# Optimization experiments

Hardware: AMD Instinct MI355X
Metric: run time of the kernel (lower is better)

## Reference

```python
import jax, jax.numpy as jnp
import numpy as np

# ---- static module configuration (mirrors __init__) ----
BIG, SMALL = 13, 3
IN_C = 256
GHOST_RATIO = 0.23
NK = -(-BIG // SMALL)                          # ceil(13/3) = 5 small kernels tile the big one
REP_N = int(IN_C * (1 - GHOST_RATIO)) // 2 * 2 # 196 channels go through the big-kernel path
GHOST_N = IN_C - REP_N                         # 60 identity (ghost) channels
OUT_N = REP_N * NK                             # grouped conv channel-multiplier output
PAD = SMALL - 1                                # conv padding = 2 -> conv output is (H+2, W+2)
CROP = SMALL // 2                              # crop to emulate padding=k//2 on the small axis
MID = BIG // 2
REAL_PAD = [MID - i * SMALL - PAD for i in range(NK)]  # [4, 1, -2, -5, -8] shift offsets
P = BIG                                        # safe zero-pad for static shift slicing
N_PATH = 2
BN_EPS = 1e-5


def _split_indices():
    # exact replication of the module's fixed random ghost/rep channel split
    np.random.seed(123)
    ghost = np.sort(np.random.choice(IN_C, GHOST_N, replace=False))
    rep = np.sort(np.array(list(set(range(IN_C)) - set(ghost.tolist())), dtype=np.int64))
    return jnp.asarray(ghost, jnp.int32), jnp.asarray(rep, jnp.int32)


def _dwconv(x, w):
    # depthwise conv with channel multiplier NK: groups = REP_N
    return jax.lax.conv_general_dilated(
        x, w, window_strides=(1, 1), padding=[(PAD, PAD), (PAD, PAD)],
        dimension_numbers=('NCHW', 'OIHW', 'NCHW'), feature_group_count=REP_N)


def _bn(x, g, b):
    # BatchNorm2d in training mode (batch statistics), matching nn.(Sync)BatchNorm forward
    m = jnp.mean(x, axis=(0, 2, 3), keepdims=True)
    v = jnp.var(x, axis=(0, 2, 3), keepdims=True)
    return (x - m) * jax.lax.rsqrt(v + BN_EPS) * g[None, :, None, None] + b[None, :, None, None]


def setup_inputs() -> dict:
    key = jax.random.key(0)
    ks = jax.random.split(key, 4)
    B, H, W = 32, 56, 56
    inputs = jax.random.normal(ks[0], (B, IN_C, H, W), jnp.float32)
    fan = SMALL * SMALL  # groups=REP_N -> in_ch/groups = 1
    std = (2.0 / fan) ** 0.5
    w1 = jax.random.normal(ks[1], (OUT_N, 1, SMALL, SMALL), jnp.float32) * std
    w2 = jax.random.normal(ks[2], (OUT_N, 1, SMALL, SMALL), jnp.float32) * std
    ghost_idx, rep_idx = _split_indices()
    ones = jnp.ones((REP_N,), jnp.float32)
    zeros = jnp.zeros((REP_N,), jnp.float32)
    return {
        'inputs': inputs, 'w1': w1, 'w2': w2,
        'g1': ones, 'b1': zeros, 'g2': ones, 'b2': zeros, 'g3': ones, 'b3': zeros,
        'ghost_idx': ghost_idx, 'rep_idx': rep_idx,
    }


def reference(inputs, w1, w2, g1, b1, g2, b2, g3, b3, ghost_idx, rep_idx):
    B, C, H, W = inputs.shape
    rep_x = jnp.take(inputs, rep_idx, axis=1)      # [B, REP_N, H, W]
    ghost_x = jnp.take(inputs, ghost_idx, axis=1)  # [B, GHOST_N, H, W]

    # N_path grouped depthwise convs summed (pre-merge branch of the module)
    out = _dwconv(rep_x, w1) + _dwconv(rep_x, w2)  # [B, REP_N*NK, H+2, W+2]
    H2, W2 = out.shape[-2:]
    # grouped conv channel order: channel c -> outputs c*NK .. c*NK+NK-1
    x = out.reshape(B, REP_N, NK, H2, W2)

    # AddShift: stack the NK small-conv responses with shifts to emulate
    # a (BIG x SMALL) kernel (shift along H) and a (SMALL x BIG) kernel (shift along W).
    lora1 = jnp.zeros((B, REP_N, H, W), out.dtype)
    lora2 = jnp.zeros((B, REP_N, H, W), out.dtype)
    for i, r in enumerate(REAL_PAD):  # NK is a small static constant
        ci = x[:, :, i]  # [B, REP_N, H2, W2]
        yh = jnp.pad(ci, ((0, 0), (0, 0), (P, P), (0, 0)))
        lora1 = lora1 + yh[:, :, P - r:P - r + H, CROP:CROP + W]
        yw = jnp.pad(ci, ((0, 0), (0, 0), (0, 0), (P, P)))
        lora2 = lora2 + yw[:, :, CROP:CROP + H, P - r:P - r + W]
    # small-kernel branch: center chunk, cropped to emulate padding=SMALL//2
    small = x[:, :, NK // 2, CROP:CROP + H, CROP:CROP + W]

    y = _bn(lora1, g1, b1) + _bn(lora2, g2, b2) + _bn(small, g3, b3) + rep_x
    return jnp.concatenate([y, ghost_x], axis=1)  # [B, IN_C, H, W]
```

## Files before the change

### kernel.cpp

```cpp
#include <hip/hip_runtime.h>


#define LSTRIDE 76
#define LROWS 70
#define LDS_FLOATS (LROWS * LSTRIDE)

__device__ __forceinline__ void load_tile(float* tile, const float* __restrict__ src, int tid) {
  #pragma unroll 1
  for (int g = tid; g < LDS_FLOATS / 4; g += 256)
    reinterpret_cast<float4*>(tile)[g] = float4{0.f, 0.f, 0.f, 0.f};
  __syncthreads();
  #pragma unroll 1
  for (int g = tid; g < 784; g += 256) {
    float4 v = reinterpret_cast<const float4*>(src)[g];
    int r = g / 14, c4 = g - r * 14;
    float* p = &tile[(r + 6) * LSTRIDE + 10 + 4 * c4];
    reinterpret_cast<float2*>(p)[0] = float2{v.x, v.y};
    reinterpret_cast<float2*>(p)[1] = float2{v.z, v.w};
  }
  __syncthreads();
}

__device__ __forceinline__ void conv_lora1(
    const float* tile, const float* wv, int h0, int w0,
    float (&a1)[4][4], float (&xc)[4][4]) {
  #pragma unroll
  for (int rr = 0; rr < 18; ++rr) {
    const float* rp = &tile[(h0 + rr) * LSTRIDE + w0 + 8];
    const float4 qa = *reinterpret_cast<const float4*>(rp);
    const float4 qb = *reinterpret_cast<const float4*>(rp + 4);
    const float xr[8] = {qa.x, qa.y, qa.z, qa.w, qb.x, qb.y, qb.z, qb.w};
    if (rr >= 6 && rr < 10) {
      #pragma unroll
      for (int dw = 0; dw < 4; ++dw) xc[rr - 6][dw] = xr[dw + 2];
    }
    #pragma unroll
    for (int dh = 0; dh < 4; ++dh) {
      const int t = rr - dh;
      if (t >= 0 && t < 15) {
        #pragma unroll
        for (int kw = 0; kw < 3; ++kw) {
          const float wgt = wv[3 * t + kw];
          #pragma unroll
          for (int dw = 0; dw < 4; ++dw)
            a1[dh][dw] = fmaf(xr[dw + kw + 1], wgt, a1[dh][dw]);
        }
      }
    }
  }
}

__device__ __forceinline__ void conv_l2s(
    const float* tile, const float* wv, int h0, int w0,
    float (&a2)[4][4], float (&a3)[4][4]) {
  #pragma unroll
  for (int rr = 0; rr < 6; ++rr) {
    const float* rp = &tile[(h0 + 5 + rr) * LSTRIDE + w0 + 4];
    #pragma unroll
    for (int g = 0; g < 5; ++g) {
      const float4 q = reinterpret_cast<const float4*>(rp)[g];
      const float xq[4] = {q.x, q.y, q.z, q.w};
      #pragma unroll
      for (int v = 0; v < 4; ++v) {
        const int vv = 4 * g + v;
        #pragma unroll
        for (int dh = 0; dh < 4; ++dh) {
          const int kh = rr - dh;
          if (kh >= 0 && kh < 3) {
            #pragma unroll
            for (int dw = 0; dw < 4; ++dw) {
              const int t = vv - dw;
              if (t >= 0 && t < 15)
                a2[dh][dw] = fmaf(xq[v], wv[(t / 3) * 9 + kh * 3 + (t % 3)], a2[dh][dw]);
              const int kw2 = vv - 5 - dw;
              if (kw2 >= 0 && kw2 < 3)
                a3[dh][dw] = fmaf(xq[v], wv[18 + kh * 3 + kw2], a3[dh][dw]);
            }
          }
        }
      }
    }
  }
}

extern "C" __global__ void sw_prep(const float* __restrict__ w1, const float* __restrict__ w2,
                                   float* __restrict__ wsum) {
  int i = blockIdx.x * 256 + threadIdx.x;
  if (i < 8820) wsum[i] = w1[i] + w2[i];
}

extern "C" __global__ __launch_bounds__(256) void sw_pass1(
    const float* __restrict__ in, const int* __restrict__ rep_idx,
    const float* __restrict__ wsum, float* __restrict__ partial) {
  __shared__ float tile[LDS_FLOATS];
  __shared__ float red[4][6];
  const int bid = blockIdx.x;
  const int c = bid >> 5, b = bid & 31;
  const int tid = threadIdx.x;
  const int src_c = rep_idx[c];
  load_tile(tile, in + (size_t)(b * 256 + src_c) * 3136, tid);
  float wv[45];
  {
    const float* wp = wsum + c * 45;
    #pragma unroll
    for (int j = 0; j < 45; ++j) wv[j] = wp[j];
  }
  float s1 = 0, q1 = 0, s2 = 0, q2 = 0, s3 = 0, q3 = 0;
  if (tid < 196) {
    const int th = tid / 14, tw = tid - th * 14;
    const int h0 = th * 4, w0 = tw * 4;
    {
      float a1[4][4] = {}, xc[4][4];
      conv_lora1(tile, wv, h0, w0, a1, xc);
      #pragma unroll
      for (int dh = 0; dh < 4; ++dh)
        #pragma unroll
        for (int dw = 0; dw < 4; ++dw) { float v = a1[dh][dw]; s1 += v; q1 = fmaf(v, v, q1); }
    }
    {
      float a2[4][4] = {}, a3[4][4] = {};
      conv_l2s(tile, wv, h0, w0, a2, a3);
      #pragma unroll
      for (int dh = 0; dh < 4; ++dh)
        #pragma unroll
        for (int dw = 0; dw < 4; ++dw) {
          float v = a2[dh][dw]; s2 += v; q2 = fmaf(v, v, q2);
          float u = a3[dh][dw]; s3 += u; q3 = fmaf(u, u, q3);
        }
    }
  }
  #pragma unroll
  for (int off = 32; off > 0; off >>= 1) {
    s1 += __shfl_down(s1, off); q1 += __shfl_down(q1, off);
    s2 += __shfl_down(s2, off); q2 += __shfl_down(q2, off);
    s3 += __shfl_down(s3, off); q3 += __shfl_down(q3, off);
  }
  const int lane = tid & 63, wid = tid >> 6;
  if (lane == 0) {
    red[wid][0] = s1; red[wid][1] = q1; red[wid][2] = s2;
    red[wid][3] = q2; red[wid][4] = s3; red[wid][5] = q3;
  }
  __syncthreads();
  if (tid < 6)
    partial[bid * 6 + tid] = red[0][tid] + red[1][tid] + red[2][tid] + red[3][tid];
}

extern "C" __global__ void sw_reduce(
    const float* __restrict__ partial,
    const float* __restrict__ g1, const float* __restrict__ b1,
    const float* __restrict__ g2, const float* __restrict__ b2,
    const float* __restrict__ g3, const float* __restrict__ b3,
    float* __restrict__ stats2) {
  const int c = blockIdx.x;
  const int tid = threadIdx.x;
  __shared__ float sm[6];
  if (tid < 6) {
    float s = 0;
    for (int b = 0; b < 32; ++b) s += partial[(c * 32 + b) * 6 + tid];
    sm[tid] = s;
  }
  __syncthreads();
  if (tid == 0) {
    const float N = 100352.f;
    float m1 = sm[0] / N, v1 = sm[1] / N - m1 * m1;
    float m2 = sm[2] / N, v2 = sm[3] / N - m2 * m2;
    float m3 = sm[4] / N, v3 = sm[5] / N - m3 * m3;
    float A1 = g1[c] * rsqrtf(v1 + 1e-5f);
    float A2 = g2[c] * rsqrtf(v2 + 1e-5f);
    float A3 = g3[c] * rsqrtf(v3 + 1e-5f);
    float K = b1[c] + b2[c] + b3[c] - m1 * A1 - m2 * A2 - m3 * A3;
    stats2[c * 4 + 0] = A1; stats2[c * 4 + 1] = A2;
    stats2[c * 4 + 2] = A3; stats2[c * 4 + 3] = K;
  }
}

extern "C" __global__ __launch_bounds__(256) void sw_pass2(
    const float* __restrict__ in, const int* __restrict__ rep_idx,
    const int* __restrict__ ghost_idx, const float* __restrict__ wsum,
    const float* __restrict__ stats2, float* __restrict__ out) {
  const int bid = blockIdx.x;
  const int tid = threadIdx.x;
  if (bid >= 6272) {
    const int g2 = bid - 6272;
    const int j = g2 >> 5, b = g2 & 31;
    const int src_c = ghost_idx[j];
    const float4* s = reinterpret_cast<const float4*>(in + (size_t)(b * 256 + src_c) * 3136);
    float4* d = reinterpret_cast<float4*>(out + ((size_t)(b * 256) + 196 + j) * 3136);
    #pragma unroll 1
    for (int g = tid; g < 784; g += 256) d[g] = s[g];
    return;
  }
  __shared__ float tile[LDS_FLOATS];
  const int c = bid >> 5, b = bid & 31;
  const int src_c = rep_idx[c];
  load_tile(tile, in + (size_t)(b * 256 + src_c) * 3136, tid);
  float wv[45];
  {
    const float* wp = wsum + c * 45;
    #pragma unroll
    for (int j = 0; j < 45; ++j) wv[j] = wp[j];
  }
  const float A1 = stats2[c * 4 + 0], A2 = stats2[c * 4 + 1];
  const float A3 = stats2[c * 4 + 2], K = stats2[c * 4 + 3];
  if (tid < 196) {
    const int th = tid / 14, tw = tid - th * 14;
    const int h0 = th * 4, w0 = tw * 4;
    float y[4][4];
    {
      float a1[4][4] = {}, xc[4][4];
      conv_lora1(tile, wv, h0, w0, a1, xc);
      #pragma unroll
      for (int dh = 0; dh < 4; ++dh)
        #pragma unroll
        for (int dw = 0; dw < 4; ++dw)
          y[dh][dw] = fmaf(A1, a1[dh][dw], K + xc[dh][dw]);
    }
    {
      float a2[4][4] = {}, a3[4][4] = {};
      conv_l2s(tile, wv, h0, w0, a2, a3);
      #pragma unroll
      for (int dh = 0; dh < 4; ++dh)
        #pragma unroll
        for (int dw = 0; dw < 4; ++dw) {
          y[dh][dw] = fmaf(A2, a2[dh][dw], y[dh][dw]);
          y[dh][dw] = fmaf(A3, a3[dh][dw], y[dh][dw]);
        }
    }
    float* op = out + ((size_t)(b * 256) + c) * 3136;
    #pragma unroll
    for (int dh = 0; dh < 4; ++dh) {
      float4 o{y[dh][0], y[dh][1], y[dh][2], y[dh][3]};
      *reinterpret_cast<float4*>(op + (h0 + dh) * 56 + w0) = o;
    }
  }
}

extern "C" void kernel_launch(void* const* d_in, const int* in_sizes, int n_in,
                              void* d_out, int out_size, void* d_ws, size_t ws_size,
                              hipStream_t stream) {
  const float* in  = (const float*)d_in[0];
  const float* w1  = (const float*)d_in[1];
  const float* w2  = (const float*)d_in[2];
  const float* g1  = (const float*)d_in[3];
  const float* b1  = (const float*)d_in[4];
  const float* g2  = (const float*)d_in[5];
  const float* b2  = (const float*)d_in[6];
  const float* g3  = (const float*)d_in[7];
  const float* b3  = (const float*)d_in[8];
  const int* ghost_idx = (const int*)d_in[9];
  const int* rep_idx   = (const int*)d_in[10];
  float* out = (float*)d_out;
  float* ws  = (float*)d_ws;

  float* wsum    = ws;
  float* stats2  = ws + 8832;
  float* partial = ws + 9728;

  sw_prep<<<35, 256, 0, stream>>>(w1, w2, wsum);
  sw_pass1<<<6272, 256, 0, stream>>>(in, rep_idx, wsum, partial);
  sw_reduce<<<196, 64, 0, stream>>>(partial, g1, b1, g2, b2, g3, b3, stats2);
  sw_pass2<<<8192, 256, 0, stream>>>(in, rep_idx, ghost_idx, wsum, stats2, out);
}
```

Measured before the change: 182.7 us.

## Replace LDS tiles with register-streamed row windows over batch-parallel threads

The convolution kernels no longer stage a padded image tile in LDS. Each 448-thread block now covers 8 output rows of one channel across all 32 batch images, one thread per batch×4-column strip. Each thread streams 22 input rows straight from global memory into a register window, using clamped indices and masks for padding, and accumulates the vertical and horizontal branches in rolling register arrays. This removes the LDS zero-fill, barriers and per-image tile setup, and cuts the partial-sum count per channel to 7. In exchange it adds redundant global loads of overlapping halo rows, higher register pressure, and a single template kernel reused for both passes.

Result: faster. 170.4 us (-6.7%).

```diff
diff --git a/kernel.cpp b/kernel.cpp
--- a/kernel.cpp
+++ b/kernel.cpp
@@ -1,84 +1,183 @@
 #include <hip/hip_runtime.h>
 
 
-#define LSTRIDE 76
-#define LROWS 70
-#define LDS_FLOATS (LROWS * LSTRIDE)
-
-__device__ __forceinline__ void load_tile(float* tile, const float* __restrict__ src, int tid) {
-  #pragma unroll 1
-  for (int g = tid; g < LDS_FLOATS / 4; g += 256)
-    reinterpret_cast<float4*>(tile)[g] = float4{0.f, 0.f, 0.f, 0.f};
-  __syncthreads();
-  #pragma unroll 1
-  for (int g = tid; g < 784; g += 256) {
-    float4 v = reinterpret_cast<const float4*>(src)[g];
-    int r = g / 14, c4 = g - r * 14;
-    float* p = &tile[(r + 6) * LSTRIDE + 10 + 4 * c4];
-    reinterpret_cast<float2*>(p)[0] = float2{v.x, v.y};
-    reinterpret_cast<float2*>(p)[1] = float2{v.z, v.w};
-  }
-  __syncthreads();
-}
-
-__device__ __forceinline__ void conv_lora1(
-    const float* tile, const float* wv, int h0, int w0,
-    float (&a1)[4][4], float (&xc)[4][4]) {
+#define B_    32
+#define CIN   256
+#define REPN  196
+#define HW    56
+#define IMG   3136
+#define NTOT  (B_ * CIN * IMG)
+#define NCONVBLK 1400
+#define NGHOSTBLK 1920
+
+template <bool PASS2>
+__launch_bounds__(448)
+__global__ void sw_conv(const float* __restrict__ in, const int* __restrict__ rep_idx,
+                        const int* __restrict__ ghost_idx, const float* __restrict__ wsum,
+                        const float* __restrict__ stats2, float* __restrict__ partial,
+                        float* __restrict__ out) {
+  const int bid = blockIdx.x;
+  const int tid = threadIdx.x;
+
+  if (PASS2 && bid >= NCONVBLK) {
+    const int g = bid - NCONVBLK;
+    const int j = g >> 5, b = g & 31;
+    const int src_c = ghost_idx[j];
+    const float4* s = reinterpret_cast<const float4*>(in + (size_t)(b * CIN + src_c) * IMG);
+    float4* d = reinterpret_cast<float4*>(out + ((size_t)(b * CIN) + REPN + j) * IMG);
+    #pragma unroll 1
+    for (int i = tid; i < 784; i += 448) d[i] = s[i];
+    return;
+  }
+
+  const int c = (bid / 56) * 8 + (bid & 7);
+  const int rb = (bid % 56) >> 3;
+  if (c >= REPN) return;
+  const int h0 = rb * 8;
+
+  const int b = tid / 14;
+  const int tw = tid - b * 14;
+  const int w0 = tw * 4;
+  const int src_c = rep_idx[c];
+  const int ibase = (b * CIN + src_c) * IMG;
+
+  float wv[45];
   #pragma unroll
-  for (int rr = 0; rr < 18; ++rr) {
-    const float* rp = &tile[(h0 + rr) * LSTRIDE + w0 + 8];
-    const float4 qa = *reinterpret_cast<const float4*>(rp);
-    const float4 qb = *reinterpret_cast<const float4*>(rp + 4);
-    const float xr[8] = {qa.x, qa.y, qa.z, qa.w, qb.x, qb.y, qb.z, qb.w};
-    if (rr >= 6 && rr < 10) {
-      #pragma unroll
-      for (int dw = 0; dw < 4; ++dw) xc[rr - 6][dw] = xr[dw + 2];
-    }
+  for (int j = 0; j < 45; ++j) wv[j] = wsum[c * 45 + j];
+
+  float A1 = 0.f, A2 = 0.f, A3 = 0.f, K_ = 0.f;
+  if (PASS2) {
+    A1 = stats2[c * 4 + 0]; A2 = stats2[c * 4 + 1];
+    A3 = stats2[c * 4 + 2]; K_ = stats2[c * 4 + 3];
+  }
+
+  const float ma = (tw >= 2) ? 1.f : 0.f;
+  const float mb = (tw >= 1) ? 1.f : 0.f;
+  const float mc = (tw <= 12) ? 1.f : 0.f;
+  const float md = (tw <= 11) ? 1.f : 0.f;
+
+  float acc1[8][4] = {};
+  float acc2[3][4] = {};
+  float acc3[3][4] = {};
+  float stash[7][4];
+  float s1 = 0, q1 = 0, s2 = 0, q2 = 0, s3 = 0, q3 = 0;
+
+  #pragma unroll
+  for (int s = 0; s < 22; ++s) {
+    const int r = h0 - 6 + s;
+    if (r >= 0 && r < HW) {
+      float win[20];
+      {
+        const int base = ibase + r * HW + w0 - 8;
+        #pragma unroll
+        for (int g = 0; g < 5; ++g) {
+          int idx = base + 4 * g;
+          idx = idx < 0 ? 0 : idx;
+          idx = idx > (NTOT - 4) ? (NTOT - 4) : idx;
+          const float4 v = *reinterpret_cast<const float4*>(in + idx);
+          win[4 * g + 0] = v.x; win[4 * g + 1] = v.y;
+          win[4 * g + 2] = v.z; win[4 * g + 3] = v.w;
+        }
+      }
+      #pragma unroll
+      for (int e = 0; e < 4; ++e) win[e] *= ma;
+      #pragma unroll
+      for (int e = 4; e < 8; ++e) win[e] *= mb;
+      #pragma unroll
+      for (int e = 12; e < 16; ++e) win[e] *= mc;
+      #pragma unroll
+      for (int e = 16; e < 20; ++e) win[e] *= md;
+
+      #pragma unroll
+      for (int lr = 0; lr < 8; ++lr) {
+        const int t = s - lr;
+        if (t >= 0 && t < 15) {
+          #pragma unroll
+          for (int kw = 0; kw < 3; ++kw) {
+            const float wgt = wv[3 * t + kw];
+            #pragma unroll
+            for (int dw = 0; dw < 4; ++dw)
+              acc1[lr][dw] = fmaf(win[dw + kw + 7], wgt, acc1[lr][dw]);
+          }
+        }
+      }
+      #pragma unroll
+      for (int lr = 0; lr < 8; ++lr) {
+        const int kh = s - lr - 5;
+        if (kh >= 0 && kh < 3) {
+          #pragma unroll
+          for (int T = 0; T < 15; ++T) {
+            const float wgt = wv[(T / 3) * 9 + kh * 3 + (T % 3)];
+            #pragma unroll
+            for (int dw = 0; dw < 4; ++dw)
+              acc2[lr % 3][dw] = fmaf(win[dw + T + 2], wgt, acc2[lr % 3][dw]);
+          }
+          #pragma unroll
+          for (int kw = 0; kw < 3; ++kw) {
+            const float wgt = wv[18 + kh * 3 + kw];
+            #pragma unroll
+            for (int dw = 0; dw < 4; ++dw)
+              acc3[lr % 3][dw] = fmaf(win[dw + kw + 7], wgt, acc3[lr % 3][dw]);
+          }
+        }
+      }
+    }
+
+    if (s >= 14) {
+      const int lr = s - 14;
+      if (PASS2) {
+        const int hh = h0 + lr;
+        const float4 xv = *reinterpret_cast<const float4*>(in + ibase + hh * HW + w0);
+        float4 o;
+        o.x = fmaf(A1, acc1[lr][0], stash[lr % 7][0] + K_ + xv.x);
+        o.y = fmaf(A1, acc1[lr][1], stash[lr % 7][1] + K_ + xv.y);
+        o.z = fmaf(A1, acc1[lr][2], stash[lr % 7][2] + K_ + xv.z);
+        o.w = fmaf(A1, acc1[lr][3], stash[lr % 7][3] + K_ + xv.w);
+        *reinterpret_cast<float4*>(out + (size_t)(b * CIN + c) * IMG + hh * HW + w0) = o;
+      } else {
+        #pragma unroll
+        for (int dw = 0; dw < 4; ++dw) {
+          const float v = acc1[lr][dw];
+          s1 += v; q1 = fmaf(v, v, q1);
+        }
+      }
+    }
+    if (s >= 7 && s <= 14) {
+      const int lr = s - 7;
+      #pragma unroll
+      for (int dw = 0; dw < 4; ++dw) {
+        const float v2 = acc2[lr % 3][dw], v3 = acc3[lr % 3][dw];
+        if (PASS2) {
+          stash[lr % 7][dw] = fmaf(A2, v2, A3 * v3);
+        } else {
+          s2 += v2; q2 = fmaf(v2, v2, q2);
+          s3 += v3; q3 = fmaf(v3, v3, q3);
+        }
+        acc2[lr % 3][dw] = 0.f;
+        acc3[lr % 3][dw] = 0.f;
+      }
+    }
+  }
+
+  if (!PASS2) {
+    __shared__ float red[7][6];
     #pragma unroll
-    for (int dh = 0; dh < 4; ++dh) {
-      const int t = rr - dh;
-      if (t >= 0 && t < 15) {
-        #pragma unroll
-        for (int kw = 0; kw < 3; ++kw) {
-          const float wgt = wv[3 * t + kw];
-          #pragma unroll
-          for (int dw = 0; dw < 4; ++dw)
-            a1[dh][dw] = fmaf(xr[dw + kw + 1], wgt, a1[dh][dw]);
-        }
-      }
-    }
-  }
-}
-
-__device__ __forceinline__ void conv_l2s(
-    const float* tile, const float* wv, int h0, int w0,
-    float (&a2)[4][4], float (&a3)[4][4]) {
-  #pragma unroll
-  for (int rr = 0; rr < 6; ++rr) {
-    const float* rp = &tile[(h0 + 5 + rr) * LSTRIDE + w0 + 4];
-    #pragma unroll
-    for (int g = 0; g < 5; ++g) {
-      const float4 q = reinterpret_cast<const float4*>(rp)[g];
-      const float xq[4] = {q.x, q.y, q.z, q.w};
-      #pragma unroll
-      for (int v = 0; v < 4; ++v) {
-        const int vv = 4 * g + v;
-        #pragma unroll
-        for (int dh = 0; dh < 4; ++dh) {
-          const int kh = rr - dh;
-          if (kh >= 0 && kh < 3) {
-            #pragma unroll
-            for (int dw = 0; dw < 4; ++dw) {
-              const int t = vv - dw;
-              if (t >= 0 && t < 15)
-                a2[dh][dw] = fmaf(xq[v], wv[(t / 3) * 9 + kh * 3 + (t % 3)], a2[dh][dw]);
-              const int kw2 = vv - 5 - dw;
-              if (kw2 >= 0 && kw2 < 3)
-                a3[dh][dw] = fmaf(xq[v], wv[18 + kh * 3 + kw2], a3[dh][dw]);
-            }
-          }
-        }
-      }
+    for (int off = 32; off > 0; off >>= 1) {
+      s1 += __shfl_down(s1, off); q1 += __shfl_down(q1, off);
+      s2 += __shfl_down(s2, off); q2 += __shfl_down(q2, off);
+      s3 += __shfl_down(s3, off); q3 += __shfl_down(q3, off);
+    }
+    const int lane = tid & 63, wid = tid >> 6;
+    if (lane == 0) {
+      red[wid][0] = s1; red[wid][1] = q1; red[wid][2] = s2;
+      red[wid][3] = q2; red[wid][4] = s3; red[wid][5] = q3;
+    }
+    __syncthreads();
+    if (tid < 6) {
+      float t = 0;
+      #pragma unroll
+      for (int w = 0; w < 7; ++w) t += red[w][tid];
+      partial[(c * 7 + rb) * 6 + tid] = t;
     }
   }
 }
@@ -87,62 +186,6 @@
                                    float* __restrict__ wsum) {
   int i = blockIdx.x * 256 + threadIdx.x;
   if (i < 8820) wsum[i] = w1[i] + w2[i];
-}
-
-extern "C" __global__ __launch_bounds__(256) void sw_pass1(
-    const float* __restrict__ in, const int* __restrict__ rep_idx,
-    const float* __restrict__ wsum, float* __restrict__ partial) {
-  __shared__ float tile[LDS_FLOATS];
-  __shared__ float red[4][6];
-  const int bid = blockIdx.x;
-  const int c = bid >> 5, b = bid & 31;
-  const int tid = threadIdx.x;
-  const int src_c = rep_idx[c];
-  load_tile(tile, in + (size_t)(b * 256 + src_c) * 3136, tid);
-  float wv[45];
-  {
-    const float* wp = wsum + c * 45;
-    #pragma unroll
-    for (int j = 0; j < 45; ++j) wv[j] = wp[j];
-  }
-  float s1 = 0, q1 = 0, s2 = 0, q2 = 0, s3 = 0, q3 = 0;
-  if (tid < 196) {
-    const int th = tid / 14, tw = tid - th * 14;
-    const int h0 = th * 4, w0 = tw * 4;
-    {
-      float a1[4][4] = {}, xc[4][4];
-      conv_lora1(tile, wv, h0, w0, a1, xc);
-      #pragma unroll
-      for (int dh = 0; dh < 4; ++dh)
-        #pragma unroll
-        for (int dw = 0; dw < 4; ++dw) { float v = a1[dh][dw]; s1 += v; q1 = fmaf(v, v, q1); }
-    }
-    {
-      float a2[4][4] = {}, a3[4][4] = {};
-      conv_l2s(tile, wv, h0, w0, a2, a3);
-      #pragma unroll
-      for (int dh = 0; dh < 4; ++dh)
-        #pragma unroll
-        for (int dw = 0; dw < 4; ++dw) {
-          float v = a2[dh][dw]; s2 += v; q2 = fmaf(v, v, q2);
-          float u = a3[dh][dw]; s3 += u; q3 = fmaf(u, u, q3);
-        }
-    }
-  }
-  #pragma unroll
-  for (int off = 32; off > 0; off >>= 1) {
-    s1 += __shfl_down(s1, off); q1 += __shfl_down(q1, off);
-    s2 += __shfl_down(s2, off); q2 += __shfl_down(q2, off);
-    s3 += __shfl_down(s3, off); q3 += __shfl_down(q3, off);
-  }
-  const int lane = tid & 63, wid = tid >> 6;
-  if (lane == 0) {
-    red[wid][0] = s1; red[wid][1] = q1; red[wid][2] = s2;
-    red[wid][3] = q2; red[wid][4] = s3; red[wid][5] = q3;
-  }
-  __syncthreads();
-  if (tid < 6)
-    partial[bid * 6 + tid] = red[0][tid] + red[1][tid] + red[2][tid] + red[3][tid];
 }
 
 extern "C" __global__ void sw_reduce(
@@ -156,7 +199,8 @@
   __shared__ float sm[6];
   if (tid < 6) {
     float s = 0;
-    for (int b = 0; b < 32; ++b) s += partial[(c * 32 + b) * 6 + tid];
+    #pragma unroll
+    for (int rb = 0; rb < 7; ++rb) s += partial[(c * 7 + rb) * 6 + tid];
     sm[tid] = s;
   }
   __syncthreads();
@@ -171,67 +215,6 @@
     float K = b1[c] + b2[c] + b3[c] - m1 * A1 - m2 * A2 - m3 * A3;
     stats2[c * 4 + 0] = A1; stats2[c * 4 + 1] = A2;
     stats2[c * 4 + 2] = A3; stats2[c * 4 + 3] = K;
-  }
-}
-
-extern "C" __global__ __launch_bounds__(256) void sw_pass2(
-    const float* __restrict__ in, const int* __restrict__ rep_idx,
-    const int* __restrict__ ghost_idx, const float* __restrict__ wsum,
-    const float* __restrict__ stats2, float* __restrict__ out) {
-  const int bid = blockIdx.x;
-  const int tid = threadIdx.x;
-  if (bid >= 6272) {
-    const int g2 = bid - 6272;
-    const int j = g2 >> 5, b = g2 & 31;
-    const int src_c = ghost_idx[j];
-    const float4* s = reinterpret_cast<const float4*>(in + (size_t)(b * 256 + src_c) * 3136);
-    float4* d = reinterpret_cast<float4*>(out + ((size_t)(b * 256) + 196 + j) * 3136);
-    #pragma unroll 1
-    for (int g = tid; g < 784; g += 256) d[g] = s[g];
-    return;
-  }
-  __shared__ float tile[LDS_FLOATS];
-  const int c = bid >> 5, b = bid & 31;
-  const int src_c = rep_idx[c];
-  load_tile(tile, in + (size_t)(b * 256 + src_c) * 3136, tid);
-  float wv[45];
-  {
-    const float* wp = wsum + c * 45;
-    #pragma unroll
-    for (int j = 0; j < 45; ++j) wv[j] = wp[j];
-  }
-  const float A1 = stats2[c * 4 + 0], A2 = stats2[c * 4 + 1];
-  const float A3 = stats2[c * 4 + 2], K = stats2[c * 4 + 3];
-  if (tid < 196) {
-    const int th = tid / 14, tw = tid - th * 14;
-    const int h0 = th * 4, w0 = tw * 4;
-    float y[4][4];
-    {
-      float a1[4][4] = {}, xc[4][4];
-      conv_lora1(tile, wv, h0, w0, a1, xc);
-      #pragma unroll
-      for (int dh = 0; dh < 4; ++dh)
-        #pragma unroll
-        for (int dw = 0; dw < 4; ++dw)
-          y[dh][dw] = fmaf(A1, a1[dh][dw], K + xc[dh][dw]);
-    }
-    {
-      float a2[4][4] = {}, a3[4][4] = {};
-      conv_l2s(tile, wv, h0, w0, a2, a3);
-      #pragma unroll
-      for (int dh = 0; dh < 4; ++dh)
-        #pragma unroll
-        for (int dw = 0; dw < 4; ++dw) {
-          y[dh][dw] = fmaf(A2, a2[dh][dw], y[dh][dw]);
-          y[dh][dw] = fmaf(A3, a3[dh][dw], y[dh][dw]);
-        }
-    }
-    float* op = out + ((size_t)(b * 256) + c) * 3136;
-    #pragma unroll
-    for (int dh = 0; dh < 4; ++dh) {
-      float4 o{y[dh][0], y[dh][1], y[dh][2], y[dh][3]};
-      *reinterpret_cast<float4*>(op + (h0 + dh) * 56 + w0) = o;
-    }
   }
 }
 
@@ -257,7 +240,7 @@
   float* partial = ws + 9728;
 
   sw_prep<<<35, 256, 0, stream>>>(w1, w2, wsum);
-  sw_pass1<<<6272, 256, 0, stream>>>(in, rep_idx, wsum, partial);
+  sw_conv<false><<<NCONVBLK, 448, 0, stream>>>(in, rep_idx, ghost_idx, wsum, stats2, partial, out);
   sw_reduce<<<196, 64, 0, stream>>>(partial, g1, b1, g2, b2, g3, b3, stats2);
-  sw_pass2<<<8192, 256, 0, stream>>>(in, rep_idx, ghost_idx, wsum, stats2, out);
-}
+  sw_conv<true><<<NCONVBLK + NGHOSTBLK, 448, 0, stream>>>(in, rep_idx, ghost_idx, wsum, stats2, partial, out);
+}
```
